# Optimization experiments

Hardware: AMD Instinct MI355X
Metric: run time of the kernel (lower is better)

Reference implementation:

```python
import jax, jax.numpy as jnp
import numpy as np

B, V, E, L, D = 16, 19, 361, 256, 64  # batch, vertices, edges/graph, seq_len, d_model
F_IN = 2 * D + 1  # concat(src_feat, tgt_feat, edge_weight)


def _linear_init(key, fan_in, fan_out):
    bound = 1.0 / np.sqrt(fan_in)
    kw, kb = jax.random.split(key)
    W = jax.random.uniform(kw, (fan_in, fan_out), jnp.float32, -bound, bound)
    b = jax.random.uniform(kb, (fan_out,), jnp.float32, -bound, bound)
    return W, b


def setup_inputs() -> dict:
    key = jax.random.key(0)
    ks = jax.random.split(key, 6)
    hidden_states = jax.random.normal(ks[0], (B * V, L, D), jnp.float32)
    edge_index = jax.random.randint(ks[1], (2, B * E, L), 0, B * V, dtype=jnp.int32)
    edge_weight = jax.random.uniform(ks[2], (B * E, L), jnp.float32)
    W1, b1 = _linear_init(ks[3], F_IN, D)
    W2, b2 = _linear_init(ks[4], D, D // 2)
    W3, b3 = _linear_init(ks[5], D // 2, 1)
    skip_param = jnp.float32(0.25)
    return {"hidden_states": hidden_states, "edge_weight": edge_weight,
            "W1": W1, "b1": b1, "W2": W2, "b2": b2, "W3": W3, "b3": b3,
            "skip_param": skip_param, "edge_index": edge_index}


def reference(hidden_states, edge_weight, W1, b1, W2, b2, W3, b3, skip_param, edge_index):
    # hidden_states: (B*V, L, D) -> (B, L, V, D) for per-timestep node gather
    hs = hidden_states.reshape(B, V, L, D).transpose(0, 2, 1, 3)
    # edge indices are global node ids; local vertex id = idx % V (as in torch code)
    src = (edge_index[0] % V).reshape(B, E, L).transpose(0, 2, 1)  # (B, L, E)
    tgt = (edge_index[1] % V).reshape(B, E, L).transpose(0, 2, 1)
    ew = edge_weight.reshape(B, E, L).transpose(0, 2, 1)           # (B, L, E)
    src_feat = jnp.take_along_axis(hs, src[..., None], axis=2)    # (B, L, E, D)
    tgt_feat = jnp.take_along_axis(hs, tgt[..., None], axis=2)    # (B, L, E, D)
    x = jnp.concatenate([src_feat, tgt_feat, ew[..., None]], axis=-1)  # (B, L, E, 2D+1)
    h = jax.nn.silu(x @ W1 + b1)
    h = jax.nn.silu(h @ W2 + b2)
    w = jax.nn.sigmoid((h @ W3 + b3)[..., 0])                     # (B, L, E)
    new_ew = skip_param * ew + (1.0 - skip_param) * w
    return new_ew.transpose(0, 2, 1).reshape(B * E, L)            # (B*E, L)
```

## Files before the change

### kernel.cpp

```cpp
#include <hip/hip_runtime.h>

#define NB 16
#define NV 19
#define NE 361
#define NL 256
#define ND 64
#define NTP 24
#define NEP (NTP * 16)
#define ATS 72

typedef __attribute__((ext_vector_type(8))) short bf16x8;
typedef __attribute__((ext_vector_type(4))) float f32x4;
typedef __attribute__((ext_vector_type(2))) __bf16 bf16v2;

union bf8u { unsigned u[4]; bf16x8 v; uint4 q; };

__device__ __forceinline__ unsigned pack_bf16(float lo, float hi) {
    bf16v2 v; v.x = (__bf16)lo; v.y = (__bf16)hi;
    return __builtin_bit_cast(unsigned, v);
}
__device__ __forceinline__ short f2bf(float f) {
    __bf16 h = (__bf16)f;
    return __builtin_bit_cast(short, h);
}
__device__ __forceinline__ f32x4 silu4(f32x4 x) {
    f32x4 t = x * -1.44269504f;
    f32x4 d;
    d.x = __builtin_amdgcn_exp2f(t.x);
    d.y = __builtin_amdgcn_exp2f(t.y);
    d.z = __builtin_amdgcn_exp2f(t.z);
    d.w = __builtin_amdgcn_exp2f(t.w);
    d += 1.f;
    f32x4 r;
    r.x = __builtin_amdgcn_rcpf(d.x);
    r.y = __builtin_amdgcn_rcpf(d.y);
    r.z = __builtin_amdgcn_rcpf(d.z);
    r.w = __builtin_amdgcn_rcpf(d.w);
    return x * r;
}
__device__ __forceinline__ float sigm(float x) {
    return __builtin_amdgcn_rcpf(1.f + __builtin_amdgcn_exp2f(x * -1.44269504f));
}

__global__ __launch_bounds__(256, 4) void edge_learner_kernel(
    const float* __restrict__ hs,
    const float* __restrict__ ew_in,
    const float* __restrict__ W1,
    const float* __restrict__ b1,
    const float* __restrict__ W2,
    const float* __restrict__ b2,
    const float* __restrict__ W3,
    const float* __restrict__ b3,
    const float* __restrict__ skip_p,
    const int*   __restrict__ eidx,
    float* __restrict__ out)
{
    __shared__ __align__(16) short A_T[64 * ATS];
    __shared__ __align__(8)  uint2 meta_s[NEP];

    const int tid  = threadIdx.x;
    const int lane = tid & 63;
    const int wave = tid >> 6;
    const int lq   = lane >> 4;
    const int lm   = lane & 15;
    const int bid0 = blockIdx.x;
    const int bid  = (bid0 & 7) * 512 + (bid0 >> 3);
    const int b    = bid >> 8;
    const int l    = bid & 255;

    for (int i = tid; i < 64 * ATS / 8; i += 256) {
        uint4 z; z.x = 0; z.y = 0; z.z = 0; z.w = 0;
        *(uint4*)&A_T[i * 8] = z;
    }

    for (int e = tid; e < NEP; e += 256) {
        uint2 m;
        if (e < NE) {
            size_t row = (size_t)(b * NE + e) * NL + l;
            unsigned s = (unsigned)(eidx[row] % NV);
            unsigned t = (unsigned)(eidx[(size_t)NB * NE * NL + row] % NV);
            m.x = s | (t << 16);
            m.y = __builtin_bit_cast(unsigned, ew_in[row]);
        } else {
            m.x = 0; m.y = 0;
        }
        meta_s[e] = m;
    }

    bf8u w2f[2][2];
    #pragma unroll
    for (int nt = 0; nt < 2; ++nt)
        #pragma unroll
        for (int ks = 0; ks < 2; ++ks) {
            const float* w2p = &W2[(ks * 32 + lq * 8) * 32 + nt * 16 + lm];
            #pragma unroll
            for (int p = 0; p < 4; ++p)
                w2f[nt][ks].u[p] = pack_bf16(w2p[(2 * p) * 32], w2p[(2 * p + 1) * 32]);
        }
    const f32x4 b2v0 = *(const f32x4*)&b2[lq * 4];
    const f32x4 b2v1 = *(const f32x4*)&b2[16 + lq * 4];
    const f32x4 w3v0 = *(const f32x4*)&W3[lq * 4];
    const f32x4 w3v1 = *(const f32x4*)&W3[16 + lq * 4];
    const float b3v  = b3[0];
    const float skip = skip_p[0];

    __syncthreads();

    if (tid < 64) A_T[tid * ATS + 31] = f2bf(W1[128 * 64 + tid]);

    {
        const int half = wave >> 1;
        const int oc0  = (wave & 1) * 32;
        const float hb0 = 0.5f * b1[(wave * 32 + lm) & 63];
        const float hb1 = 0.5f * b1[(wave * 32 + 16 + lm) & 63];
        bf8u w1f[2][2];
        #pragma unroll
        for (int nt = 0; nt < 2; ++nt)
            #pragma unroll
            for (int ks = 0; ks < 2; ++ks) {
                const float* wp = &W1[(half * 64 + ks * 32 + lq * 8) * 64
                                      + oc0 + nt * 16 + lm];
                #pragma unroll
                for (int p = 0; p < 4; ++p)
                    w1f[nt][ks].u[p] = pack_bf16(wp[(2 * p) * 64], wp[(2 * p + 1) * 64]);
            }

        f32x4 acc00 = {0,0,0,0}, acc01 = {0,0,0,0}, acc10 = {0,0,0,0}, acc11 = {0,0,0,0};
        #pragma unroll
        for (int Mt = 0; Mt < 2; ++Mt) {
            int v  = Mt * 16 + lm;
            int vc = v < NV ? v : NV - 1;
            const float* hp = hs + ((size_t)(b * NV + vc) * NL + l) * ND;
            bf8u af[2];
            #pragma unroll
            for (int ks = 0; ks < 2; ++ks) {
                float4 x0 = *(const float4*)&hp[ks * 32 + lq * 8];
                float4 x1 = *(const float4*)&hp[ks * 32 + lq * 8 + 4];
                af[ks].u[0] = pack_bf16(x0.x, x0.y);
                af[ks].u[1] = pack_bf16(x0.z, x0.w);
                af[ks].u[2] = pack_bf16(x1.x, x1.y);
                af[ks].u[3] = pack_bf16(x1.z, x1.w);
            }
            if (Mt == 0) {
                acc00 = __builtin_amdgcn_mfma_f32_16x16x32_bf16(af[0].v, w1f[0][0].v, acc00, 0, 0, 0);
                acc00 = __builtin_amdgcn_mfma_f32_16x16x32_bf16(af[1].v, w1f[0][1].v, acc00, 0, 0, 0);
                acc01 = __builtin_amdgcn_mfma_f32_16x16x32_bf16(af[0].v, w1f[1][0].v, acc01, 0, 0, 0);
                acc01 = __builtin_amdgcn_mfma_f32_16x16x32_bf16(af[1].v, w1f[1][1].v, acc01, 0, 0, 0);
            } else {
                acc10 = __builtin_amdgcn_mfma_f32_16x16x32_bf16(af[0].v, w1f[0][0].v, acc10, 0, 0, 0);
                acc10 = __builtin_amdgcn_mfma_f32_16x16x32_bf16(af[1].v, w1f[0][1].v, acc10, 0, 0, 0);
                acc11 = __builtin_amdgcn_mfma_f32_16x16x32_bf16(af[0].v, w1f[1][0].v, acc11, 0, 0, 0);
                acc11 = __builtin_amdgcn_mfma_f32_16x16x32_bf16(af[1].v, w1f[1][1].v, acc11, 0, 0, 0);
            }
        }
        const int tr0 = (wave & 1) * 32 + lm;
        const int tr1 = (wave & 1) * 32 + 16 + lm;
        const int cof = (wave >> 1) * 32;
        #pragma unroll
        for (int r = 0; r < 4; ++r) {
            int v0 = lq * 4 + r;
            A_T[tr0 * ATS + cof + v0] = f2bf(acc00[r] + hb0);
            A_T[tr1 * ATS + cof + v0] = f2bf(acc01[r] + hb1);
            int v1 = 16 + lq * 4 + r;
            if (v1 < NV) {
                A_T[tr0 * ATS + cof + v1] = f2bf(acc10[r] + hb0);
                A_T[tr1 * ATS + cof + v1] = f2bf(acc11[r] + hb1);
            }
        }
    }
    __syncthreads();

    bf8u afr[4][2];
    #pragma unroll
    for (int mt = 0; mt < 4; ++mt) {
        const int c = (mt >> 1) * 32 + (mt & 1) * 4 + ((lm >> 2) << 3) + (lm & 3);
        #pragma unroll
        for (int kc = 0; kc < 2; ++kc)
            afr[mt][kc].q = *(const uint4*)&A_T[c * ATS + kc * 32 + lq * 8];
    }

    uint2 mr[6];
    #pragma unroll
    for (int i = 0; i < 6; ++i)
        mr[i] = meta_s[(wave + 4 * i) * 16 + lm];

    #pragma unroll
    for (int i = 0; i < 6; ++i) {
        const int t = wave + 4 * i;
        const int src = (int)(mr[i].x & 0xffffu);
        const int tgt = (int)(mr[i].x >> 16);
        const float ew = __builtin_bit_cast(float, mr[i].y);

        bf8u s0, s1;
        {
            const int base = lq * 8;
            int w  = src - base;
            int ix = w >> 1;
            unsigned pat = (w & 1) ? 0x3F800000u : 0x3F80u;
            s0.u[0] = (ix == 0) ? pat : 0u;
            s0.u[1] = (ix == 1) ? pat : 0u;
            s0.u[2] = (ix == 2) ? pat : 0u;
            s0.u[3] = (ix == 3) ? pat : 0u;
            unsigned ewm = (lq == 3) ? (((unsigned)(unsigned short)f2bf(ew)) << 16) : 0u;
            s0.u[3] |= ewm;
            int w2_ = tgt - base;
            int ix2 = w2_ >> 1;
            unsigned pat2 = (w2_ & 1) ? 0x3F800000u : 0x3F80u;
            s1.u[0] = (ix2 == 0) ? pat2 : 0u;
            s1.u[1] = (ix2 == 1) ? pat2 : 0u;
            s1.u[2] = (ix2 == 2) ? pat2 : 0u;
            s1.u[3] = (ix2 == 3) ? pat2 : 0u;
        }

        __builtin_amdgcn_s_setprio(1);
        f32x4 z0 = {0,0,0,0}, z1 = {0,0,0,0}, z2 = {0,0,0,0}, z3 = {0,0,0,0};
        z0 = __builtin_amdgcn_mfma_f32_16x16x32_bf16(afr[0][0].v, s0.v, z0, 0, 0, 0);
        z0 = __builtin_amdgcn_mfma_f32_16x16x32_bf16(afr[0][1].v, s1.v, z0, 0, 0, 0);
        z1 = __builtin_amdgcn_mfma_f32_16x16x32_bf16(afr[1][0].v, s0.v, z1, 0, 0, 0);
        z1 = __builtin_amdgcn_mfma_f32_16x16x32_bf16(afr[1][1].v, s1.v, z1, 0, 0, 0);
        z2 = __builtin_amdgcn_mfma_f32_16x16x32_bf16(afr[2][0].v, s0.v, z2, 0, 0, 0);
        z2 = __builtin_amdgcn_mfma_f32_16x16x32_bf16(afr[2][1].v, s1.v, z2, 0, 0, 0);
        z3 = __builtin_amdgcn_mfma_f32_16x16x32_bf16(afr[3][0].v, s0.v, z3, 0, 0, 0);
        z3 = __builtin_amdgcn_mfma_f32_16x16x32_bf16(afr[3][1].v, s1.v, z3, 0, 0, 0);
        __builtin_amdgcn_s_setprio(0);

        f32x4 y0 = silu4(z0), y1 = silu4(z1), y2 = silu4(z2), y3 = silu4(z3);
        bf8u a1[2];
        a1[0].u[0] = pack_bf16(y0.x, y0.y);
        a1[0].u[1] = pack_bf16(y0.z, y0.w);
        a1[0].u[2] = pack_bf16(y1.x, y1.y);
        a1[0].u[3] = pack_bf16(y1.z, y1.w);
        a1[1].u[0] = pack_bf16(y2.x, y2.y);
        a1[1].u[1] = pack_bf16(y2.z, y2.w);
        a1[1].u[2] = pack_bf16(y3.x, y3.y);
        a1[1].u[3] = pack_bf16(y3.z, y3.w);

        __builtin_amdgcn_s_setprio(1);
        f32x4 c0 = {0,0,0,0}, c1 = {0,0,0,0};
        c0 = __builtin_amdgcn_mfma_f32_16x16x32_bf16(w2f[0][0].v, a1[0].v, c0, 0, 0, 0);
        c0 = __builtin_amdgcn_mfma_f32_16x16x32_bf16(w2f[0][1].v, a1[1].v, c0, 0, 0, 0);
        c1 = __builtin_amdgcn_mfma_f32_16x16x32_bf16(w2f[1][0].v, a1[0].v, c1, 0, 0, 0);
        c1 = __builtin_amdgcn_mfma_f32_16x16x32_bf16(w2f[1][1].v, a1[1].v, c1, 0, 0, 0);
        __builtin_amdgcn_s_setprio(0);

        f32x4 h0 = silu4(c0 + b2v0);
        f32x4 h1 = silu4(c1 + b2v1);
        f32x4 pv = h0 * w3v0 + h1 * w3v1;
        float p  = (pv.x + pv.y) + (pv.z + pv.w);
        p += __shfl_xor(p, 16);
        p += __shfl_xor(p, 32);

        if (lane < 16) {
            int er = t * 16 + lane;
            if (er < NE) {
                float wgt = sigm(p + b3v);
                out[(size_t)(b * NE + er) * NL + l] = skip * ew + (1.f - skip) * wgt;
            }
        }
    }
}

extern "C" void kernel_launch(void* const* d_in, const int* in_sizes, int n_in,
                              void* d_out, int out_size, void* d_ws, size_t ws_size,
                              hipStream_t stream) {
    const float* hs   = (const float*)d_in[0];
    const float* ew   = (const float*)d_in[1];
    const float* W1   = (const float*)d_in[2];
    const float* b1   = (const float*)d_in[3];
    const float* W2   = (const float*)d_in[4];
    const float* b2   = (const float*)d_in[5];
    const float* W3   = (const float*)d_in[6];
    const float* b3   = (const float*)d_in[7];
    const float* skip = (const float*)d_in[8];
    const int*   eidx = (const int*)d_in[9];
    float* outp = (float*)d_out;

    dim3 grid(NB * NL);
    dim3 block(256);
    hipLaunchKernelGGL(edge_learner_kernel, grid, block, 0, stream,
                       hs, ew, W1, b1, W2, b2, W3, b3, skip, eidx, outp);
}
```

Before: 57.83 us.

## Process four timesteps per block, amortizing weight setup and prefetching edge metadata

Each block now handles four consecutive timesteps instead of one, so the grid shrinks by four and the W1/W2 fragment loads and bf16 packing run once per four timesteps. Edge metadata for the next timestep is loaded into shared memory while the current timestep's MLP runs, with an extra barrier per iteration. The s_setprio hints around the MFMA blocks are dropped. The cost is fewer blocks (1024) and therefore less parallelism across CUs, and the global loads of edge indices are now serialized inside each block.

```diff
diff --git a/kernel.cpp b/kernel.cpp
--- a/kernel.cpp
+++ b/kernel.cpp
@@ -5,9 +5,9 @@
 #define NE 361
 #define NL 256
 #define ND 64
-#define NTP 24
-#define NEP (NTP * 16)
+#define NEP 384
 #define ATS 72
+#define NPP 4
 
 typedef __attribute__((ext_vector_type(8))) short bf16x8;
 typedef __attribute__((ext_vector_type(4))) float f32x4;
@@ -64,9 +64,10 @@
     const int lq   = lane >> 4;
     const int lm   = lane & 15;
     const int bid0 = blockIdx.x;
-    const int bid  = (bid0 & 7) * 512 + (bid0 >> 3);
-    const int b    = bid >> 8;
-    const int l    = bid & 255;
+    const int bid  = (bid0 & 7) * 128 + (bid0 >> 3);
+    const int plb  = bid * NPP;
+    const int b    = plb >> 8;
+    const int l0   = plb & 255;
 
     for (int i = tid; i < 64 * ATS / 8; i += 256) {
         uint4 z; z.x = 0; z.y = 0; z.z = 0; z.w = 0;
@@ -76,7 +77,7 @@
     for (int e = tid; e < NEP; e += 256) {
         uint2 m;
         if (e < NE) {
-            size_t row = (size_t)(b * NE + e) * NL + l;
+            size_t row = (size_t)(b * NE + e) * NL + l0;
             unsigned s = (unsigned)(eidx[row] % NV);
             unsigned t = (unsigned)(eidx[(size_t)NB * NE * NL + row] % NV);
             m.x = s | (t << 16);
@@ -104,157 +105,176 @@
     const float b3v  = b3[0];
     const float skip = skip_p[0];
 
+    const int half = wave >> 1;
+    const int oc0  = (wave & 1) * 32;
+    const float hb0 = 0.5f * b1[(wave * 32 + lm) & 63];
+    const float hb1 = 0.5f * b1[(wave * 32 + 16 + lm) & 63];
+    bf8u w1f[2][2];
+    #pragma unroll
+    for (int nt = 0; nt < 2; ++nt)
+        #pragma unroll
+        for (int ks = 0; ks < 2; ++ks) {
+            const float* wp = &W1[(half * 64 + ks * 32 + lq * 8) * 64
+                                  + oc0 + nt * 16 + lm];
+            #pragma unroll
+            for (int p = 0; p < 4; ++p)
+                w1f[nt][ks].u[p] = pack_bf16(wp[(2 * p) * 64], wp[(2 * p + 1) * 64]);
+        }
+
     __syncthreads();
 
     if (tid < 64) A_T[tid * ATS + 31] = f2bf(W1[128 * 64 + tid]);
 
-    {
-        const int half = wave >> 1;
-        const int oc0  = (wave & 1) * 32;
-        const float hb0 = 0.5f * b1[(wave * 32 + lm) & 63];
-        const float hb1 = 0.5f * b1[(wave * 32 + 16 + lm) & 63];
-        bf8u w1f[2][2];
-        #pragma unroll
-        for (int nt = 0; nt < 2; ++nt)
-            #pragma unroll
-            for (int ks = 0; ks < 2; ++ks) {
-                const float* wp = &W1[(half * 64 + ks * 32 + lq * 8) * 64
-                                      + oc0 + nt * 16 + lm];
+    #pragma unroll 1
+    for (int it = 0; it < NPP; ++it) {
+        const int l = l0 + it;
+
+        {
+            f32x4 acc00 = {0,0,0,0}, acc01 = {0,0,0,0},
+                  acc10 = {0,0,0,0}, acc11 = {0,0,0,0};
+            #pragma unroll
+            for (int Mt = 0; Mt < 2; ++Mt) {
+                int v  = Mt * 16 + lm;
+                int vc = v < NV ? v : NV - 1;
+                const float* hp = hs + ((size_t)(b * NV + vc) * NL + l) * ND;
+                bf8u af[2];
                 #pragma unroll
-                for (int p = 0; p < 4; ++p)
-                    w1f[nt][ks].u[p] = pack_bf16(wp[(2 * p) * 64], wp[(2 * p + 1) * 64]);
-            }
-
-        f32x4 acc00 = {0,0,0,0}, acc01 = {0,0,0,0}, acc10 = {0,0,0,0}, acc11 = {0,0,0,0};
-        #pragma unroll
-        for (int Mt = 0; Mt < 2; ++Mt) {
-            int v  = Mt * 16 + lm;
-            int vc = v < NV ? v : NV - 1;
-            const float* hp = hs + ((size_t)(b * NV + vc) * NL + l) * ND;
-            bf8u af[2];
-            #pragma unroll
-            for (int ks = 0; ks < 2; ++ks) {
-                float4 x0 = *(const float4*)&hp[ks * 32 + lq * 8];
-                float4 x1 = *(const float4*)&hp[ks * 32 + lq * 8 + 4];
-                af[ks].u[0] = pack_bf16(x0.x, x0.y);
-                af[ks].u[1] = pack_bf16(x0.z, x0.w);
-                af[ks].u[2] = pack_bf16(x1.x, x1.y);
-                af[ks].u[3] = pack_bf16(x1.z, x1.w);
-            }
-            if (Mt == 0) {
-                acc00 = __builtin_amdgcn_mfma_f32_16x16x32_bf16(af[0].v, w1f[0][0].v, acc00, 0, 0, 0);
-                acc00 = __builtin_amdgcn_mfma_f32_16x16x32_bf16(af[1].v, w1f[0][1].v, acc00, 0, 0, 0);
-                acc01 = __builtin_amdgcn_mfma_f32_16x16x32_bf16(af[0].v, w1f[1][0].v, acc01, 0, 0, 0);
-                acc01 = __builtin_amdgcn_mfma_f32_16x16x32_bf16(af[1].v, w1f[1][1].v, acc01, 0, 0, 0);
-            } else {
-                acc10 = __builtin_amdgcn_mfma_f32_16x16x32_bf16(af[0].v, w1f[0][0].v, acc10, 0, 0, 0);
-                acc10 = __builtin_amdgcn_mfma_f32_16x16x32_bf16(af[1].v, w1f[0][1].v, acc10, 0, 0, 0);
-                acc11 = __builtin_amdgcn_mfma_f32_16x16x32_bf16(af[0].v, w1f[1][0].v, acc11, 0, 0, 0);
-                acc11 = __builtin_amdgcn_mfma_f32_16x16x32_bf16(af[1].v, w1f[1][1].v, acc11, 0, 0, 0);
-            }
-        }
-        const int tr0 = (wave & 1) * 32 + lm;
-        const int tr1 = (wave & 1) * 32 + 16 + lm;
-        const int cof = (wave >> 1) * 32;
-        #pragma unroll
-        for (int r = 0; r < 4; ++r) {
-            int v0 = lq * 4 + r;
-            A_T[tr0 * ATS + cof + v0] = f2bf(acc00[r] + hb0);
-            A_T[tr1 * ATS + cof + v0] = f2bf(acc01[r] + hb1);
-            int v1 = 16 + lq * 4 + r;
-            if (v1 < NV) {
-                A_T[tr0 * ATS + cof + v1] = f2bf(acc10[r] + hb0);
-                A_T[tr1 * ATS + cof + v1] = f2bf(acc11[r] + hb1);
-            }
-        }
-    }
-    __syncthreads();
-
-    bf8u afr[4][2];
-    #pragma unroll
-    for (int mt = 0; mt < 4; ++mt) {
-        const int c = (mt >> 1) * 32 + (mt & 1) * 4 + ((lm >> 2) << 3) + (lm & 3);
-        #pragma unroll
-        for (int kc = 0; kc < 2; ++kc)
-            afr[mt][kc].q = *(const uint4*)&A_T[c * ATS + kc * 32 + lq * 8];
-    }
-
-    uint2 mr[6];
-    #pragma unroll
-    for (int i = 0; i < 6; ++i)
-        mr[i] = meta_s[(wave + 4 * i) * 16 + lm];
-
-    #pragma unroll
-    for (int i = 0; i < 6; ++i) {
-        const int t = wave + 4 * i;
-        const int src = (int)(mr[i].x & 0xffffu);
-        const int tgt = (int)(mr[i].x >> 16);
-        const float ew = __builtin_bit_cast(float, mr[i].y);
-
-        bf8u s0, s1;
-        {
-            const int base = lq * 8;
-            int w  = src - base;
-            int ix = w >> 1;
-            unsigned pat = (w & 1) ? 0x3F800000u : 0x3F80u;
-            s0.u[0] = (ix == 0) ? pat : 0u;
-            s0.u[1] = (ix == 1) ? pat : 0u;
-            s0.u[2] = (ix == 2) ? pat : 0u;
-            s0.u[3] = (ix == 3) ? pat : 0u;
-            unsigned ewm = (lq == 3) ? (((unsigned)(unsigned short)f2bf(ew)) << 16) : 0u;
-            s0.u[3] |= ewm;
-            int w2_ = tgt - base;
-            int ix2 = w2_ >> 1;
-            unsigned pat2 = (w2_ & 1) ? 0x3F800000u : 0x3F80u;
-            s1.u[0] = (ix2 == 0) ? pat2 : 0u;
-            s1.u[1] = (ix2 == 1) ? pat2 : 0u;
-            s1.u[2] = (ix2 == 2) ? pat2 : 0u;
-            s1.u[3] = (ix2 == 3) ? pat2 : 0u;
-        }
-
-        __builtin_amdgcn_s_setprio(1);
-        f32x4 z0 = {0,0,0,0}, z1 = {0,0,0,0}, z2 = {0,0,0,0}, z3 = {0,0,0,0};
-        z0 = __builtin_amdgcn_mfma_f32_16x16x32_bf16(afr[0][0].v, s0.v, z0, 0, 0, 0);
-        z0 = __builtin_amdgcn_mfma_f32_16x16x32_bf16(afr[0][1].v, s1.v, z0, 0, 0, 0);
-        z1 = __builtin_amdgcn_mfma_f32_16x16x32_bf16(afr[1][0].v, s0.v, z1, 0, 0, 0);
-        z1 = __builtin_amdgcn_mfma_f32_16x16x32_bf16(afr[1][1].v, s1.v, z1, 0, 0, 0);
-        z2 = __builtin_amdgcn_mfma_f32_16x16x32_bf16(afr[2][0].v, s0.v, z2, 0, 0, 0);
-        z2 = __builtin_amdgcn_mfma_f32_16x16x32_bf16(afr[2][1].v, s1.v, z2, 0, 0, 0);
-        z3 = __builtin_amdgcn_mfma_f32_16x16x32_bf16(afr[3][0].v, s0.v, z3, 0, 0, 0);
-        z3 = __builtin_amdgcn_mfma_f32_16x16x32_bf16(afr[3][1].v, s1.v, z3, 0, 0, 0);
-        __builtin_amdgcn_s_setprio(0);
-
-        f32x4 y0 = silu4(z0), y1 = silu4(z1), y2 = silu4(z2), y3 = silu4(z3);
-        bf8u a1[2];
-        a1[0].u[0] = pack_bf16(y0.x, y0.y);
-        a1[0].u[1] = pack_bf16(y0.z, y0.w);
-        a1[0].u[2] = pack_bf16(y1.x, y1.y);
-        a1[0].u[3] = pack_bf16(y1.z, y1.w);
-        a1[1].u[0] = pack_bf16(y2.x, y2.y);
-        a1[1].u[1] = pack_bf16(y2.z, y2.w);
-        a1[1].u[2] = pack_bf16(y3.x, y3.y);
-        a1[1].u[3] = pack_bf16(y3.z, y3.w);
-
-        __builtin_amdgcn_s_setprio(1);
-        f32x4 c0 = {0,0,0,0}, c1 = {0,0,0,0};
-        c0 = __builtin_amdgcn_mfma_f32_16x16x32_bf16(w2f[0][0].v, a1[0].v, c0, 0, 0, 0);
-        c0 = __builtin_amdgcn_mfma_f32_16x16x32_bf16(w2f[0][1].v, a1[1].v, c0, 0, 0, 0);
-        c1 = __builtin_amdgcn_mfma_f32_16x16x32_bf16(w2f[1][0].v, a1[0].v, c1, 0, 0, 0);
-        c1 = __builtin_amdgcn_mfma_f32_16x16x32_bf16(w2f[1][1].v, a1[1].v, c1, 0, 0, 0);
-        __builtin_amdgcn_s_setprio(0);
-
-        f32x4 h0 = silu4(c0 + b2v0);
-        f32x4 h1 = silu4(c1 + b2v1);
-        f32x4 pv = h0 * w3v0 + h1 * w3v1;
-        float p  = (pv.x + pv.y) + (pv.z + pv.w);
-        p += __shfl_xor(p, 16);
-        p += __shfl_xor(p, 32);
-
-        if (lane < 16) {
-            int er = t * 16 + lane;
-            if (er < NE) {
-                float wgt = sigm(p + b3v);
-                out[(size_t)(b * NE + er) * NL + l] = skip * ew + (1.f - skip) * wgt;
+                for (int ks = 0; ks < 2; ++ks) {
+                    float4 x0 = *(const float4*)&hp[ks * 32 + lq * 8];
+                    float4 x1 = *(const float4*)&hp[ks * 32 + lq * 8 + 4];
+                    af[ks].u[0] = pack_bf16(x0.x, x0.y);
+                    af[ks].u[1] = pack_bf16(x0.z, x0.w);
+                    af[ks].u[2] = pack_bf16(x1.x, x1.y);
+                    af[ks].u[3] = pack_bf16(x1.z, x1.w);
+                }
+                if (Mt == 0) {
+                    acc00 = __builtin_amdgcn_mfma_f32_16x16x32_bf16(af[0].v, w1f[0][0].v, acc00, 0, 0, 0);
+                    acc00 = __builtin_amdgcn_mfma_f32_16x16x32_bf16(af[1].v, w1f[0][1].v, acc00, 0, 0, 0);
+                    acc01 = __builtin_amdgcn_mfma_f32_16x16x32_bf16(af[0].v, w1f[1][0].v, acc01, 0, 0, 0);
+                    acc01 = __builtin_amdgcn_mfma_f32_16x16x32_bf16(af[1].v, w1f[1][1].v, acc01, 0, 0, 0);
+                } else {
+                    acc10 = __builtin_amdgcn_mfma_f32_16x16x32_bf16(af[0].v, w1f[0][0].v, acc10, 0, 0, 0);
+                    acc10 = __builtin_amdgcn_mfma_f32_16x16x32_bf16(af[1].v, w1f[0][1].v, acc10, 0, 0, 0);
+                    acc11 = __builtin_amdgcn_mfma_f32_16x16x32_bf16(af[0].v, w1f[1][0].v, acc11, 0, 0, 0);
+                    acc11 = __builtin_amdgcn_mfma_f32_16x16x32_bf16(af[1].v, w1f[1][1].v, acc11, 0, 0, 0);
+                }
+            }
+            const int tr0 = (wave & 1) * 32 + lm;
+            const int tr1 = (wave & 1) * 32 + 16 + lm;
+            const int cof = (wave >> 1) * 32;
+            #pragma unroll
+            for (int r = 0; r < 4; ++r) {
+                int v0 = lq * 4 + r;
+                A_T[tr0 * ATS + cof + v0] = f2bf(acc00[r] + hb0);
+                A_T[tr1 * ATS + cof + v0] = f2bf(acc01[r] + hb1);
+                int v1 = 16 + lq * 4 + r;
+                if (v1 < NV) {
+                    A_T[tr0 * ATS + cof + v1] = f2bf(acc10[r] + hb0);
+                    A_T[tr1 * ATS + cof + v1] = f2bf(acc11[r] + hb1);
+                }
+            }
+        }
+        __syncthreads();
+
+        bf8u afr[4][2];
+        #pragma unroll
+        for (int mt = 0; mt < 4; ++mt) {
+            const int c = (mt >> 1) * 32 + (mt & 1) * 4 + ((lm >> 2) << 3) + (lm & 3);
+            #pragma unroll
+            for (int kc = 0; kc < 2; ++kc)
+                afr[mt][kc].q = *(const uint4*)&A_T[c * ATS + kc * 32 + lq * 8];
+        }
+        uint2 mr[6];
+        #pragma unroll
+        for (int i = 0; i < 6; ++i)
+            mr[i] = meta_s[(wave + 4 * i) * 16 + lm];
+        __syncthreads();
+
+        if (it < NPP - 1) {
+            const int ln = l + 1;
+            for (int e = tid; e < NEP; e += 256) {
+                uint2 m;
+                if (e < NE) {
+                    size_t row = (size_t)(b * NE + e) * NL + ln;
+                    unsigned s = (unsigned)(eidx[row] % NV);
+                    unsigned t = (unsigned)(eidx[(size_t)NB * NE * NL + row] % NV);
+                    m.x = s | (t << 16);
+                    m.y = __builtin_bit_cast(unsigned, ew_in[row]);
+                } else {
+                    m.x = 0; m.y = 0;
+                }
+                meta_s[e] = m;
+            }
+        }
+
+        #pragma unroll
+        for (int i = 0; i < 6; ++i) {
+            const int t = wave + 4 * i;
+            const int src = (int)(mr[i].x & 0xffffu);
+            const int tgt = (int)(mr[i].x >> 16);
+            const float ew = __builtin_bit_cast(float, mr[i].y);
+
+            bf8u s0, s1;
+            {
+                const int base = lq * 8;
+                int w  = src - base;
+                int ix = w >> 1;
+                unsigned pat = (w & 1) ? 0x3F800000u : 0x3F80u;
+                s0.u[0] = (ix == 0) ? pat : 0u;
+                s0.u[1] = (ix == 1) ? pat : 0u;
+                s0.u[2] = (ix == 2) ? pat : 0u;
+                s0.u[3] = (ix == 3) ? pat : 0u;
+                unsigned ewm = (lq == 3) ? (((unsigned)(unsigned short)f2bf(ew)) << 16) : 0u;
+                s0.u[3] |= ewm;
+                int w2_ = tgt - base;
+                int ix2 = w2_ >> 1;
+                unsigned pat2 = (w2_ & 1) ? 0x3F800000u : 0x3F80u;
+                s1.u[0] = (ix2 == 0) ? pat2 : 0u;
+                s1.u[1] = (ix2 == 1) ? pat2 : 0u;
+                s1.u[2] = (ix2 == 2) ? pat2 : 0u;
+                s1.u[3] = (ix2 == 3) ? pat2 : 0u;
+            }
+
+            f32x4 z0 = {0,0,0,0}, z1 = {0,0,0,0}, z2 = {0,0,0,0}, z3 = {0,0,0,0};
+            z0 = __builtin_amdgcn_mfma_f32_16x16x32_bf16(afr[0][0].v, s0.v, z0, 0, 0, 0);
+            z0 = __builtin_amdgcn_mfma_f32_16x16x32_bf16(afr[0][1].v, s1.v, z0, 0, 0, 0);
+            z1 = __builtin_amdgcn_mfma_f32_16x16x32_bf16(afr[1][0].v, s0.v, z1, 0, 0, 0);
+            z1 = __builtin_amdgcn_mfma_f32_16x16x32_bf16(afr[1][1].v, s1.v, z1, 0, 0, 0);
+            z2 = __builtin_amdgcn_mfma_f32_16x16x32_bf16(afr[2][0].v, s0.v, z2, 0, 0, 0);
+            z2 = __builtin_amdgcn_mfma_f32_16x16x32_bf16(afr[2][1].v, s1.v, z2, 0, 0, 0);
+            z3 = __builtin_amdgcn_mfma_f32_16x16x32_bf16(afr[3][0].v, s0.v, z3, 0, 0, 0);
+            z3 = __builtin_amdgcn_mfma_f32_16x16x32_bf16(afr[3][1].v, s1.v, z3, 0, 0, 0);
+
+            f32x4 y0 = silu4(z0), y1 = silu4(z1), y2 = silu4(z2), y3 = silu4(z3);
+            bf8u a1[2];
+            a1[0].u[0] = pack_bf16(y0.x, y0.y);
+            a1[0].u[1] = pack_bf16(y0.z, y0.w);
+            a1[0].u[2] = pack_bf16(y1.x, y1.y);
+            a1[0].u[3] = pack_bf16(y1.z, y1.w);
+            a1[1].u[0] = pack_bf16(y2.x, y2.y);
+            a1[1].u[1] = pack_bf16(y2.z, y2.w);
+            a1[1].u[2] = pack_bf16(y3.x, y3.y);
+            a1[1].u[3] = pack_bf16(y3.z, y3.w);
+
+            f32x4 c0 = {0,0,0,0}, c1 = {0,0,0,0};
+            c0 = __builtin_amdgcn_mfma_f32_16x16x32_bf16(w2f[0][0].v, a1[0].v, c0, 0, 0, 0);
+            c0 = __builtin_amdgcn_mfma_f32_16x16x32_bf16(w2f[0][1].v, a1[1].v, c0, 0, 0, 0);
+            c1 = __builtin_amdgcn_mfma_f32_16x16x32_bf16(w2f[1][0].v, a1[0].v, c1, 0, 0, 0);
+            c1 = __builtin_amdgcn_mfma_f32_16x16x32_bf16(w2f[1][1].v, a1[1].v, c1, 0, 0, 0);
+
+            f32x4 h0 = silu4(c0 + b2v0);
+            f32x4 h1 = silu4(c1 + b2v1);
+            f32x4 pv = h0 * w3v0 + h1 * w3v1;
+            float p  = (pv.x + pv.y) + (pv.z + pv.w);
+            p += __shfl_xor(p, 16);
+            p += __shfl_xor(p, 32);
+
+            if (lane < 16) {
+                int er = t * 16 + lane;
+                if (er < NE) {
+                    float wgt = sigm(p + b3v);
+                    out[(size_t)(b * NE + er) * NL + l] = skip * ew + (1.f - skip) * wgt;
+                }
             }
         }
     }
@@ -275,7 +295,7 @@
     const int*   eidx = (const int*)d_in[9];
     float* outp = (float*)d_out;
 
-    dim3 grid(NB * NL);
+    dim3 grid(NB * NL / NPP);
     dim3 block(256);
     hipLaunchKernelGGL(edge_learner_kernel, grid, block, 0, stream,
                        hs, ew, W1, b1, W2, b2, W3, b3, skip, eidx, outp);
```

Result: slower. 74.10 us (+28.1%).
